# Kernel tuning notes

Hardware: AMD Instinct MI355X
Metric: run time of the kernel (lower is better)

The kernel has to match this reference:

```python
import jax, jax.numpy as jnp
import numpy as np

D = 2048   # embed_dim
E = 128    # expand_ratio = head dim
H = D // E # num heads = 16
C = 64     # chunk size for the chunked linear-attention scan
EPS = 1e-6


def setup_inputs() -> dict:
    key = jax.random.key(0)
    ks = jax.random.split(key, 6)
    b, n = 2, 2048
    s = 0.02
    x = jax.random.normal(ks[0], (b, n, D), jnp.float32)
    Wq = (jax.random.normal(ks[1], (D, D), jnp.float32) * s)
    Wk = (jax.random.normal(ks[2], (D, D), jnp.float32) * s)
    Wv = (jax.random.normal(ks[3], (D, D), jnp.float32) * s)
    Wf = (jax.random.normal(ks[4], (D, H), jnp.float32) * s)
    Wo = (jax.random.normal(ks[5], (D, D), jnp.float32) * s)
    norm_w = jnp.ones((D,), jnp.float32)
    return {"x": x, "Wq": Wq, "Wk": Wk, "Wv": Wv, "Wf": Wf, "Wo": Wo, "norm_w": norm_w}


def _lightning_scalar_decay(q, k, v, ld):
    # q,k,v: [b,n,H,E], ld: [b,n,H] log decay per head per step.
    # Recurrence: S_t = exp(ld_t) * S_{t-1} + k_t^T v_t ; o_t = q_t @ S_t
    b, n, h, e = q.shape
    nc = n // C
    qc = q.reshape(b, nc, C, h, e)
    kc = k.reshape(b, nc, C, h, e)
    vc = v.reshape(b, nc, C, h, e)
    ldc = ld.reshape(b, nc, C, h)
    cum = jnp.cumsum(ldc, axis=2)          # inclusive within-chunk log decay [b,nc,C,h]
    tot = cum[:, :, -1, :]                 # [b,nc,h]

    # intra-chunk: scores[i,j] = (q_i . k_j) * exp(L_i - L_j), j <= i
    Lh = cum.transpose(0, 1, 3, 2)         # [b,nc,h,C]
    decay = jnp.exp(Lh[..., :, None] - Lh[..., None, :])  # [b,nc,h,C,C]
    mask = jnp.tril(jnp.ones((C, C), bool))
    scores = jnp.einsum('bmihe,bmjhe->bmhij', qc, kc) * decay
    scores = jnp.where(mask, scores, 0.0)
    o_intra = jnp.einsum('bmhij,bmjhe->bmihe', scores, vc)

    # inter-chunk: carried recurrent state S [b,h,e,e]
    def step(S, inp):
        q_c, k_c, v_c, cum_c, tot_c = inp  # [b,C,h,e],...,[b,C,h],[b,h]
        o = jnp.einsum('bihe,bhef->bihf', q_c * jnp.exp(cum_c)[..., None], S)
        kd = k_c * jnp.exp(tot_c[:, None, :] - cum_c)[..., None]
        S_new = S * jnp.exp(tot_c)[:, :, None, None] + jnp.einsum('bihe,bihf->bhef', kd, v_c)
        return S_new, o

    xs = (qc.transpose(1, 0, 2, 3, 4), kc.transpose(1, 0, 2, 3, 4),
          vc.transpose(1, 0, 2, 3, 4), cum.transpose(1, 0, 2, 3), tot.transpose(1, 0, 2))
    S0 = jnp.zeros((b, h, e, e), q.dtype)
    S_final, o_inter = jax.lax.scan(step, S0, xs)
    o_inter = o_inter.transpose(1, 0, 2, 3, 4)  # [b,nc,C,h,e]
    return (o_intra + o_inter).reshape(b, n, h * e), S_final


def reference(x, Wq, Wk, Wv, Wf, Wo, norm_w):
    b, n, d = x.shape
    q = jax.nn.silu(x @ Wq).reshape(b, n, H, E)
    k = jax.nn.silu(x @ Wk).reshape(b, n, H, E)
    v = (x @ Wv).reshape(b, n, H, E)
    ld = jax.nn.log_sigmoid(x @ Wf)  # [b,n,H]
    o, _ = _lightning_scalar_decay(q, k, v, ld)
    # RMSNorm over full embed dim
    o = o * jax.lax.rsqrt(jnp.mean(o * o, axis=-1, keepdims=True) + EPS) * norm_w
    return o @ Wo
```

## Files before the change

### kernel.cpp

```cpp
#include <hip/hip_runtime.h>
#include <hip/hip_bf16.h>
#include <stdint.h>

#define D_ 2048
#define E_ 128
#define H_ 16
#define NB_ 2
#define NSEQ_ 2048
#define NTOK_ 4096
#define NCH_ 32

typedef short bf16s;
typedef __attribute__((ext_vector_type(8))) short bf16x8;
typedef __attribute__((ext_vector_type(4))) float f32x4;

__device__ __forceinline__ short f2b(float f) {
  __hip_bfloat16 h = __float2bfloat16(f);
  return *reinterpret_cast<short*>(&h);
}
__device__ __forceinline__ float b2f(short s) {
  __hip_bfloat16 h;
  *reinterpret_cast<short*>(&h) = s;
  return __bfloat162float(h);
}

__device__ __forceinline__ void gload_lds16(const void* g, void* l) {
  __builtin_amdgcn_global_load_lds(
      (__attribute__((address_space(1))) void*)(const_cast<void*>(g)),
      (__attribute__((address_space(3))) void*)(l), 16, 0, 0);
}

__global__ __launch_bounds__(256)
void cvt_bf16(const float* __restrict__ x, bf16s* __restrict__ y) {
  const size_t i = (size_t)blockIdx.x * 256 + threadIdx.x;
  const float4 a = ((const float4*)x)[i * 2];
  const float4 b = ((const float4*)x)[i * 2 + 1];
  bf16x8 o;
  o[0] = f2b(a.x); o[1] = f2b(a.y); o[2] = f2b(a.z); o[3] = f2b(a.w);
  o[4] = f2b(b.x); o[5] = f2b(b.y); o[6] = f2b(b.z); o[7] = f2b(b.w);
  *(bf16x8*)&y[i * 8] = o;
}

__global__ __launch_bounds__(256)
void transpose_w(const float* __restrict__ Wq, const float* __restrict__ Wk,
                 const float* __restrict__ Wv, const float* __restrict__ Wo,
                 const float* __restrict__ nw, bf16s* __restrict__ WqT,
                 bf16s* __restrict__ WkT, bf16s* __restrict__ WvT,
                 bf16s* __restrict__ WoT) {
  const float* src; bf16s* dst;
  if (blockIdx.z == 0)      { src = Wq; dst = WqT; }
  else if (blockIdx.z == 1) { src = Wk; dst = WkT; }
  else if (blockIdx.z == 2) { src = Wv; dst = WvT; }
  else                      { src = Wo; dst = WoT; }
  __shared__ float tile[64][65];
  const int n0 = blockIdx.x * 64, k0 = blockIdx.y * 64;
  const int t = threadIdx.x;
  const int tr = t >> 6, tc = t & 63;
#pragma unroll
  for (int rr = 0; rr < 16; ++rr) {
    const int row = rr * 4 + tr;
    tile[row][tc] = src[(size_t)(k0 + row) * D_ + n0 + tc];
  }
  __syncthreads();
  const float wk = (blockIdx.z == 3) ? nw[k0 + tc] : 1.f;
#pragma unroll
  for (int rr = 0; rr < 16; ++rr) {
    const int row = rr * 4 + tr;
    dst[(size_t)(n0 + row) * D_ + k0 + tc] = f2b(tile[tc][row] * wk);
  }
}

__global__ __launch_bounds__(256)
void ld_gemm(const float* __restrict__ x, const float* __restrict__ Wf,
             float* __restrict__ ldb) {
  const int t = threadIdx.x;
  const int col = t & 15;
  const int tok = blockIdx.x * 16 + (t >> 4);
  const float4* xr = (const float4*)(x + (size_t)tok * D_);
  float s = 0.f;
#pragma unroll 4
  for (int kk = 0; kk < D_ / 4; ++kk) {
    const float4 xv = xr[kk];
    const int k4 = kk * 4;
    s += xv.x * Wf[(k4 + 0) * H_ + col];
    s += xv.y * Wf[(k4 + 1) * H_ + col];
    s += xv.z * Wf[(k4 + 2) * H_ + col];
    s += xv.w * Wf[(k4 + 3) * H_ + col];
  }
  const float m = fminf(s, 0.f);
  ldb[(size_t)tok * H_ + col] = m - log1pf(__expf(-fabsf(s)));
}

template <typename OT>
__device__ __forceinline__ void gemm_body(const bf16s* __restrict__ A,
                                          const bf16s* __restrict__ Bt,
                                          OT* __restrict__ Cm, int bm, int bn,
                                          int act, const float* __restrict__ rs) {
  constexpr int BK = 32;
  __shared__ bf16s As[128 * BK];
  __shared__ bf16s Bs[128 * BK];
  const int t = threadIdx.x;
  const int w = t >> 6, l = t & 63;
  const int wm = w >> 1, wn = w & 1;
  const int lr = l & 15, lk = l >> 4;
  const int sr4 = l >> 2, sc = l & 3;
  f32x4 acc[4][4] = {};

  const size_t abase = (size_t)(bm * 128) * D_;
  const size_t bbase = (size_t)(bn * 128) * D_;

  for (int k0 = 0; k0 < D_; k0 += BK) {
    __syncthreads();
#pragma unroll
    for (int j = 0; j < 2; ++j) {
      const int row0 = j * 64 + w * 16;
      const int row = row0 + sr4;
      const int cs = sc ^ ((row >> 1) & 3);
      gload_lds16(&A[abase + (size_t)row * D_ + k0 + cs * 8], &As[row0 * BK]);
      gload_lds16(&Bt[bbase + (size_t)row * D_ + k0 + cs * 8], &Bs[row0 * BK]);
    }
    __syncthreads();
    bf16x8 af[4], bfr[4];
#pragma unroll
    for (int tm = 0; tm < 4; ++tm) {
      const int row = wm * 64 + tm * 16 + lr;
      af[tm] = *(const bf16x8*)&As[row * BK + (lk ^ ((row >> 1) & 3)) * 8];
    }
#pragma unroll
    for (int tn = 0; tn < 4; ++tn) {
      const int row = wn * 64 + tn * 16 + lr;
      bfr[tn] = *(const bf16x8*)&Bs[row * BK + (lk ^ ((row >> 1) & 3)) * 8];
    }
#pragma unroll
    for (int tm = 0; tm < 4; ++tm)
#pragma unroll
      for (int tn = 0; tn < 4; ++tn)
        acc[tm][tn] = __builtin_amdgcn_mfma_f32_16x16x32_bf16(
            af[tm], bfr[tn], acc[tm][tn], 0, 0, 0);
  }

#pragma unroll
  for (int tm = 0; tm < 4; ++tm) {
    const int rowb = bm * 128 + wm * 64 + tm * 16 + lk * 4;
#pragma unroll
    for (int tn = 0; tn < 4; ++tn) {
      const int col = bn * 128 + wn * 64 + tn * 16 + lr;
#pragma unroll
      for (int r = 0; r < 4; ++r) {
        float vv = acc[tm][tn][r];
        if (act) vv = vv / (1.f + __expf(-vv));
        if constexpr (sizeof(OT) == 2) {
          Cm[(size_t)(rowb + r) * D_ + col] = f2b(vv);
        } else {
          vv *= rs[rowb + r];
          Cm[(size_t)(rowb + r) * D_ + col] = vv;
        }
      }
    }
  }
}

__global__ __launch_bounds__(256, 4)
void gemm_qkv(const bf16s* __restrict__ xb, const bf16s* __restrict__ WqT,
              const bf16s* __restrict__ WkT, const bf16s* __restrict__ WvT,
              bf16s* __restrict__ qb, bf16s* __restrict__ kb,
              bf16s* __restrict__ vb) {
  const int orig = blockIdx.x;
  const int lin = (orig & 7) * 192 + (orig >> 3);
  const int bm = lin & 31;
  const int bnz = lin >> 5;
  const int z = bnz >> 4, bn = bnz & 15;
  const bf16s* Bt; bf16s* out; int act;
  if (z == 0)      { Bt = WqT; out = qb; act = 1; }
  else if (z == 1) { Bt = WkT; out = kb; act = 1; }
  else             { Bt = WvT; out = vb; act = 0; }
  gemm_body<bf16s>(xb, Bt, out, bm, bn, act, nullptr);
}

__global__ __launch_bounds__(256, 4)
void gemm_out(const bf16s* __restrict__ A, const bf16s* __restrict__ Bt,
              const float* __restrict__ rs, float* __restrict__ out) {
  const int orig = blockIdx.x;
  const int lin = (orig & 7) * 64 + (orig >> 3);
  const int bm = lin & 31;
  const int bn = lin >> 5;
  gemm_body<float>(A, Bt, out, bm, bn, 0, rs);
}

__global__ __launch_bounds__(256)
void chunk_state(const bf16s* __restrict__ k, const bf16s* __restrict__ v,
                 const float* __restrict__ ldp, bf16s* __restrict__ Mbuf,
                 float* __restrict__ totb) {
  const int c = blockIdx.x, bh = blockIdx.y;
  const int b = bh >> 4, h = bh & 15;
  const int t = threadIdx.x;
  const int w = t >> 6, l = t & 63;
  const int lr = l & 15, lk = l >> 4;

  __shared__ bf16s Kt[64 * 128];
  __shared__ bf16s Vn[64 * 128];
  __shared__ bf16s KdT[128 * 64];
  __shared__ bf16s VtT[128 * 64];
  __shared__ float cumS[64];
  char* cKt = (char*)Kt; char* cVn = (char*)Vn;
  char* cKdT = (char*)KdT; char* cVtT = (char*)VtT;

  const size_t grow0 = (size_t)b * NSEQ_ + c * 64;
#pragma unroll
  for (int j = 0; j < 4; ++j) {
    const int lrow = w * 16 + j * 4 + (l >> 4);
    const int ck = (l & 15) ^ (lrow & 7);
    const size_t goff = (grow0 + lrow) * D_ + h * E_ + ck * 8;
    const int lbase = (w * 16 + j * 4) * 128;
    gload_lds16(&k[goff], &Kt[lbase]);
    gload_lds16(&v[goff], &Vn[lbase]);
  }
  if (w == 0) {
    float val = ldp[(grow0 + l) * H_ + h];
#pragma unroll
    for (int off = 1; off < 64; off <<= 1) {
      float pv = __shfl_up(val, off);
      if (l >= off) val += pv;
    }
    cumS[l] = val;
  }
  __syncthreads();
  const float tot = cumS[63];
  if (t == 0) totb[bh * NCH_ + c] = tot;

#pragma unroll
  for (int it = 0; it < 4; ++it) {
    const int task = t + it * 256;
    const int i = task >> 4, cx = task & 15;
    const int sb = i * 256 + ((cx * 16) ^ ((i & 7) << 4));
    bf16x8 vv = *(const bf16x8*)(cVn + sb);
    bf16x8 kk8 = *(const bf16x8*)(cKt + sb);
    const float sE = __expf(tot - cumS[i]);
#pragma unroll
    for (int jj = 0; jj < 8; ++jj) {
      const int e = cx * 8 + jj;
      const int db = e * 128 + ((i * 2) ^ ((e & 7) << 4));
      *(bf16s*)(cVtT + db) = vv[jj];
      *(bf16s*)(cKdT + db) = f2b(b2f(kk8[jj]) * sE);
    }
  }
  __syncthreads();

  const int wm = w >> 1, wn = w & 1;
  f32x4 acc[4][4] = {};
#pragma unroll
  for (int kk2 = 0; kk2 < 2; ++kk2) {
    const int cb = (kk2 * 32 + lk * 8) * 2;
    bf16x8 af[4], bfr[4];
#pragma unroll
    for (int tm = 0; tm < 4; ++tm) {
      const int fr = wm * 64 + tm * 16 + lr;
      af[tm] = *(const bf16x8*)(cVtT + fr * 128 + (cb ^ ((fr & 7) << 4)));
    }
#pragma unroll
    for (int tn = 0; tn < 4; ++tn) {
      const int er = wn * 64 + tn * 16 + lr;
      bfr[tn] = *(const bf16x8*)(cKdT + er * 128 + (cb ^ ((er & 7) << 4)));
    }
#pragma unroll
    for (int tm = 0; tm < 4; ++tm)
#pragma unroll
      for (int tn = 0; tn < 4; ++tn)
        acc[tm][tn] = __builtin_amdgcn_mfma_f32_16x16x32_bf16(
            af[tm], bfr[tn], acc[tm][tn], 0, 0, 0);
  }
  const size_t mb = (size_t)(bh * NCH_ + c) * 128 * 128;
#pragma unroll
  for (int tm = 0; tm < 4; ++tm) {
#pragma unroll
    for (int tn = 0; tn < 4; ++tn) {
#pragma unroll
      for (int r = 0; r < 4; ++r) {
        const int f = wm * 64 + tm * 16 + lk * 4 + r;
        const int e = wn * 64 + tn * 16 + lr;
        Mbuf[mb + f * 128 + e] = f2b(acc[tm][tn][r]);
      }
    }
  }
}

__global__ __launch_bounds__(256)
void state_scan(const bf16s* __restrict__ Mbuf, const float* __restrict__ totb,
                bf16s* __restrict__ Sbuf) {
  const int sl = blockIdx.x;
  const int bh = blockIdx.y;
  const int t = threadIdx.x;
  const int fr = sl * 16 + (t >> 4);
  const int e0 = (t & 15) * 8;
  const size_t base = ((size_t)(bh * NCH_) * 128 + fr) * 128 + e0;
  const size_t cstride = 128 * 128;
  __shared__ float tots[NCH_];
  if (t < NCH_) tots[t] = totb[bh * NCH_ + t];
  __syncthreads();
  float acc[8] = {};
  bf16x8 m0 = *(const bf16x8*)&Mbuf[base + 0 * cstride];
  bf16x8 m1 = *(const bf16x8*)&Mbuf[base + 1 * cstride];
  bf16x8 m2 = *(const bf16x8*)&Mbuf[base + 2 * cstride];
  bf16x8 m3 = *(const bf16x8*)&Mbuf[base + 3 * cstride];
#pragma unroll
  for (int c = 0; c < NCH_; ++c) {
    bf16x8 sv;
#pragma unroll
    for (int j = 0; j < 8; ++j) sv[j] = f2b(acc[j]);
    *(bf16x8*)&Sbuf[base + (size_t)c * cstride] = sv;
    const bf16x8 mc = ((c & 3) == 0) ? m0 : ((c & 3) == 1) ? m1
                     : ((c & 3) == 2) ? m2 : m3;
    const float dt = __expf(tots[c]);
#pragma unroll
    for (int j = 0; j < 8; ++j) acc[j] = acc[j] * dt + b2f(mc[j]);
    if (c + 4 < NCH_) {
      const bf16x8 mn = *(const bf16x8*)&Mbuf[base + (size_t)(c + 4) * cstride];
      if ((c & 3) == 0) m0 = mn;
      else if ((c & 3) == 1) m1 = mn;
      else if ((c & 3) == 2) m2 = mn;
      else m3 = mn;
    }
  }
}

__global__ __launch_bounds__(256)
void attn_out(const bf16s* __restrict__ q, const bf16s* __restrict__ k,
              const bf16s* __restrict__ v, const float* __restrict__ ldp,
              const bf16s* __restrict__ Sbuf, bf16s* __restrict__ o) {
  const int c = blockIdx.x, bh = blockIdx.y;
  const int b = bh >> 4, h = bh & 15;
  const int t = threadIdx.x;
  const int w = t >> 6, l = t & 63;
  const int lr = l & 15, lk = l >> 4;

  __shared__ bf16s Qt[64 * 128];
  __shared__ bf16s Kt[64 * 128];
  __shared__ bf16s Vn[64 * 128];
  __shared__ bf16s VtT[128 * 64];
  __shared__ bf16s Pm[64 * 64];
  __shared__ float cumS[64];
  char* cQt = (char*)Qt; char* cKt = (char*)Kt; char* cVn = (char*)Vn;
  char* cVtT = (char*)VtT; char* cPm = (char*)Pm;

  const size_t grow0 = (size_t)b * NSEQ_ + c * 64;
  const size_t sbase = (size_t)(bh * NCH_ + c) * 128 * 128;
  const bf16x8* Sp = (const bf16x8*)&Sbuf[sbase];
#pragma unroll
  for (int j = 0; j < 4; ++j) {
    const int lrow = w * 16 + j * 4 + (l >> 4);
    const int ck = (l & 15) ^ (lrow & 7);
    const size_t goff = (grow0 + lrow) * D_ + h * E_ + ck * 8;
    const int lbase = (w * 16 + j * 4) * 128;
    gload_lds16(&q[goff], &Qt[lbase]);
    gload_lds16(&k[goff], &Kt[lbase]);
    gload_lds16(&v[goff], &Vn[lbase]);
  }
  if (w == 0) {
    float val = ldp[(grow0 + l) * H_ + h];
#pragma unroll
    for (int off = 1; off < 64; off <<= 1) {
      float pv = __shfl_up(val, off);
      if (l >= off) val += pv;
    }
    cumS[l] = val;
  }
  __syncthreads();

#pragma unroll
  for (int it = 0; it < 4; ++it) {
    const int task = t + it * 256;
    const int i = task >> 4, cx = task & 15;
    const int sb = i * 256 + ((cx * 16) ^ ((i & 7) << 4));
    bf16x8 vv = *(const bf16x8*)(cVn + sb);
#pragma unroll
    for (int jj = 0; jj < 8; ++jj) {
      const int e = cx * 8 + jj;
      const int db = e * 128 + ((i * 2) ^ ((e & 7) << 4));
      *(bf16s*)(cVtT + db) = vv[jj];
    }
  }

  f32x4 accs[4] = {};
  f32x4 acco[8] = {};
#pragma unroll
  for (int kk = 0; kk < 4; ++kk) {
    const int cb = (kk * 32 + lk * 8) * 2;
    const int ar = w * 16 + lr;
    bf16x8 aq = *(const bf16x8*)(cQt + ar * 256 + (cb ^ ((ar & 7) << 4)));
#pragma unroll
    for (int tn = 0; tn < 4; ++tn) {
      const int br = tn * 16 + lr;
      bf16x8 bk = *(const bf16x8*)(cKt + br * 256 + (cb ^ ((br & 7) << 4)));
      accs[tn] = __builtin_amdgcn_mfma_f32_16x16x32_bf16(aq, bk, accs[tn], 0, 0, 0);
    }
#pragma unroll
    for (int tf = 0; tf < 8; ++tf) {
      bf16x8 bs = Sp[(tf * 16 + lr) * 16 + kk * 4 + lk];
      acco[tf] = __builtin_amdgcn_mfma_f32_16x16x32_bf16(aq, bs, acco[tf], 0, 0, 0);
    }
  }
#pragma unroll
  for (int r = 0; r < 4; ++r) {
    const float gI = __expf(cumS[w * 16 + lk * 4 + r]);
#pragma unroll
    for (int tf = 0; tf < 8; ++tf) acco[tf][r] *= gI;
  }
#pragma unroll
  for (int tn = 0; tn < 4; ++tn) {
    const int j = tn * 16 + lr;
    const float cj = cumS[j];
#pragma unroll
    for (int r = 0; r < 4; ++r) {
      const int i = w * 16 + lk * 4 + r;
      const float sv = (j <= i) ? accs[tn][r] * __expf(cumS[i] - cj) : 0.f;
      *(bf16s*)(cPm + i * 128 + ((j * 2) ^ ((i & 7) << 4))) = f2b(sv);
    }
  }
  __syncthreads();

#pragma unroll
  for (int kk2 = 0; kk2 < 2; ++kk2) {
    const int cb = (kk2 * 32 + lk * 8) * 2;
    const int pr = w * 16 + lr;
    bf16x8 ap = *(const bf16x8*)(cPm + pr * 128 + (cb ^ ((pr & 7) << 4)));
#pragma unroll
    for (int tf = 0; tf < 8; ++tf) {
      const int fr = tf * 16 + lr;
      bf16x8 bv = *(const bf16x8*)(cVtT + fr * 128 + (cb ^ ((fr & 7) << 4)));
      acco[tf] = __builtin_amdgcn_mfma_f32_16x16x32_bf16(ap, bv, acco[tf], 0, 0, 0);
    }
  }
#pragma unroll
  for (int tf = 0; tf < 8; ++tf) {
#pragma unroll
    for (int r = 0; r < 4; ++r) {
      const int i = w * 16 + lk * 4 + r;
      o[(grow0 + i) * D_ + h * E_ + tf * 16 + lr] = f2b(acco[tf][r]);
    }
  }
}

__global__ __launch_bounds__(256)
void rms_scale(const bf16s* __restrict__ o, float* __restrict__ sout) {
  const int tok = blockIdx.x;
  const int t = threadIdx.x;
  bf16x8 vv = *(const bf16x8*)&o[(size_t)tok * D_ + t * 8];
  float s = 0.f;
#pragma unroll
  for (int j = 0; j < 8; ++j) { const float f = b2f(vv[j]); s += f * f; }
#pragma unroll
  for (int off2 = 32; off2 > 0; off2 >>= 1) s += __shfl_down(s, off2);
  __shared__ float wsum[4];
  if ((t & 63) == 0) wsum[t >> 6] = s;
  __syncthreads();
  if (t == 0)
    sout[tok] = rsqrtf((wsum[0] + wsum[1] + wsum[2] + wsum[3]) * (1.f / D_) +
                       1e-6f);
}

extern "C" void kernel_launch(void* const* d_in, const int* in_sizes, int n_in,
                              void* d_out, int out_size, void* d_ws,
                              size_t ws_size, hipStream_t stream) {
  (void)in_sizes; (void)n_in; (void)out_size;
  const float* x  = (const float*)d_in[0];
  const float* Wq = (const float*)d_in[1];
  const float* Wk = (const float*)d_in[2];
  const float* Wv = (const float*)d_in[3];
  const float* Wf = (const float*)d_in[4];
  const float* Wo = (const float*)d_in[5];
  const float* nw = (const float*)d_in[6];
  float* out = (float*)d_out;

  char* ws = (char*)d_ws;
  const size_t MB = 1024 * 1024;
  bf16s* xb   = (bf16s*)(ws + 0);
  bf16s* WqT  = (bf16s*)(ws + 16 * MB);
  bf16s* WkT  = (bf16s*)(ws + 24 * MB);
  bf16s* WvT  = (bf16s*)(ws + 32 * MB);
  bf16s* Sbuf = (bf16s*)(ws + 0);
  float* totb = (float*)(ws + 32 * MB);
  bf16s* WoT  = (bf16s*)(ws + 40 * MB);
  bf16s* qb   = (bf16s*)(ws + 48 * MB);
  bf16s* kb   = (bf16s*)(ws + 64 * MB);
  bf16s* vb   = (bf16s*)(ws + 80 * MB);
  bf16s* ob   = (bf16s*)(ws + 96 * MB);
  bf16s* Mbuf = (bf16s*)(ws + 112 * MB);
  float* ldb  = (float*)(ws + 144 * MB);
  float* rsb  = (float*)(ws + 145 * MB);
  if (146 * MB > ws_size) return;

  cvt_bf16<<<NTOK_ * D_ / 8 / 256, 256, 0, stream>>>(x, xb);
  transpose_w<<<dim3(32, 32, 4), 256, 0, stream>>>(Wq, Wk, Wv, Wo, nw, WqT,
                                                   WkT, WvT, WoT);
  ld_gemm<<<NTOK_ / 16, 256, 0, stream>>>(x, Wf, ldb);
  gemm_qkv<<<1536, 256, 0, stream>>>(xb, WqT, WkT, WvT, qb, kb, vb);
  chunk_state<<<dim3(NCH_, NB_ * H_), 256, 0, stream>>>(kb, vb, ldb, Mbuf, totb);
  state_scan<<<dim3(8, NB_ * H_), 256, 0, stream>>>(Mbuf, totb, Sbuf);
  attn_out<<<dim3(NCH_, NB_ * H_), 256, 0, stream>>>(qb, kb, vb, ldb, Sbuf, ob);
  rms_scale<<<NTOK_, 256, 0, stream>>>(ob, rsb);
  gemm_out<<<512, 256, 0, stream>>>(ob, WoT, rsb, out);
}
```

Measured before the change: 317.9 us.

## Enlarge GEMM tiles to 128x256 with each wave covering all rows

The shared GEMM body now computes 128x256 output tiles. Each of the four waves handles a 128x64 slab, with 8x4 MFMA accumulators per lane instead of 4x4. This raises MFMA work per LDS fragment load and halves the block count. In exchange it doubles register use, lowers the occupancy bound to 2, and replaces the swizzled block ordering with a plain grid, which may hurt L2 locality and wave-level parallelism.

Measured after the change: 361.0 us. +13.6%, slower.

```diff
diff --git a/kernel.cpp b/kernel.cpp
--- a/kernel.cpp
+++ b/kernel.cpp
@@ -98,16 +98,15 @@
                                           int act, const float* __restrict__ rs) {
   constexpr int BK = 32;
   __shared__ bf16s As[128 * BK];
-  __shared__ bf16s Bs[128 * BK];
+  __shared__ bf16s Bs[256 * BK];
   const int t = threadIdx.x;
   const int w = t >> 6, l = t & 63;
-  const int wm = w >> 1, wn = w & 1;
   const int lr = l & 15, lk = l >> 4;
   const int sr4 = l >> 2, sc = l & 3;
-  f32x4 acc[4][4] = {};
+  f32x4 acc[8][4] = {};
 
   const size_t abase = (size_t)(bm * 128) * D_;
-  const size_t bbase = (size_t)(bn * 128) * D_;
+  const size_t bbase = (size_t)(bn * 256) * D_;
 
   for (int k0 = 0; k0 < D_; k0 += BK) {
     __syncthreads();
@@ -117,22 +116,28 @@
       const int row = row0 + sr4;
       const int cs = sc ^ ((row >> 1) & 3);
       gload_lds16(&A[abase + (size_t)row * D_ + k0 + cs * 8], &As[row0 * BK]);
+    }
+#pragma unroll
+    for (int j = 0; j < 4; ++j) {
+      const int row0 = j * 64 + w * 16;
+      const int row = row0 + sr4;
+      const int cs = sc ^ ((row >> 1) & 3);
       gload_lds16(&Bt[bbase + (size_t)row * D_ + k0 + cs * 8], &Bs[row0 * BK]);
     }
     __syncthreads();
-    bf16x8 af[4], bfr[4];
-#pragma unroll
-    for (int tm = 0; tm < 4; ++tm) {
-      const int row = wm * 64 + tm * 16 + lr;
+    bf16x8 af[8], bfr[4];
+#pragma unroll
+    for (int tm = 0; tm < 8; ++tm) {
+      const int row = tm * 16 + lr;
       af[tm] = *(const bf16x8*)&As[row * BK + (lk ^ ((row >> 1) & 3)) * 8];
     }
 #pragma unroll
     for (int tn = 0; tn < 4; ++tn) {
-      const int row = wn * 64 + tn * 16 + lr;
+      const int row = w * 64 + tn * 16 + lr;
       bfr[tn] = *(const bf16x8*)&Bs[row * BK + (lk ^ ((row >> 1) & 3)) * 8];
     }
 #pragma unroll
-    for (int tm = 0; tm < 4; ++tm)
+    for (int tm = 0; tm < 8; ++tm)
 #pragma unroll
       for (int tn = 0; tn < 4; ++tn)
         acc[tm][tn] = __builtin_amdgcn_mfma_f32_16x16x32_bf16(
@@ -140,11 +145,11 @@
   }
 
 #pragma unroll
-  for (int tm = 0; tm < 4; ++tm) {
-    const int rowb = bm * 128 + wm * 64 + tm * 16 + lk * 4;
+  for (int tm = 0; tm < 8; ++tm) {
+    const int rowb = bm * 128 + tm * 16 + lk * 4;
 #pragma unroll
     for (int tn = 0; tn < 4; ++tn) {
-      const int col = bn * 128 + wn * 64 + tn * 16 + lr;
+      const int col = bn * 256 + w * 64 + tn * 16 + lr;
 #pragma unroll
       for (int r = 0; r < 4; ++r) {
         float vv = acc[tm][tn][r];
@@ -160,16 +165,12 @@
   }
 }
 
-__global__ __launch_bounds__(256, 4)
+__global__ __launch_bounds__(256, 2)
 void gemm_qkv(const bf16s* __restrict__ xb, const bf16s* __restrict__ WqT,
               const bf16s* __restrict__ WkT, const bf16s* __restrict__ WvT,
               bf16s* __restrict__ qb, bf16s* __restrict__ kb,
               bf16s* __restrict__ vb) {
-  const int orig = blockIdx.x;
-  const int lin = (orig & 7) * 192 + (orig >> 3);
-  const int bm = lin & 31;
-  const int bnz = lin >> 5;
-  const int z = bnz >> 4, bn = bnz & 15;
+  const int bn = blockIdx.x, bm = blockIdx.y, z = blockIdx.z;
   const bf16s* Bt; bf16s* out; int act;
   if (z == 0)      { Bt = WqT; out = qb; act = 1; }
   else if (z == 1) { Bt = WkT; out = kb; act = 1; }
@@ -177,14 +178,10 @@
   gemm_body<bf16s>(xb, Bt, out, bm, bn, act, nullptr);
 }
 
-__global__ __launch_bounds__(256, 4)
+__global__ __launch_bounds__(256, 2)
 void gemm_out(const bf16s* __restrict__ A, const bf16s* __restrict__ Bt,
               const float* __restrict__ rs, float* __restrict__ out) {
-  const int orig = blockIdx.x;
-  const int lin = (orig & 7) * 64 + (orig >> 3);
-  const int bm = lin & 31;
-  const int bn = lin >> 5;
-  gemm_body<float>(A, Bt, out, bm, bn, 0, rs);
+  gemm_body<float>(A, Bt, out, blockIdx.y, blockIdx.x, 0, rs);
 }
 
 __global__ __launch_bounds__(256)
@@ -493,10 +490,10 @@
   transpose_w<<<dim3(32, 32, 4), 256, 0, stream>>>(Wq, Wk, Wv, Wo, nw, WqT,
                                                    WkT, WvT, WoT);
   ld_gemm<<<NTOK_ / 16, 256, 0, stream>>>(x, Wf, ldb);
-  gemm_qkv<<<1536, 256, 0, stream>>>(xb, WqT, WkT, WvT, qb, kb, vb);
+  gemm_qkv<<<dim3(8, 32, 3), 256, 0, stream>>>(xb, WqT, WkT, WvT, qb, kb, vb);
   chunk_state<<<dim3(NCH_, NB_ * H_), 256, 0, stream>>>(kb, vb, ldb, Mbuf, totb);
   state_scan<<<dim3(8, NB_ * H_), 256, 0, stream>>>(Mbuf, totb, Sbuf);
   attn_out<<<dim3(NCH_, NB_ * H_), 256, 0, stream>>>(qb, kb, vb, ldb, Sbuf, ob);
   rms_scale<<<NTOK_, 256, 0, stream>>>(ob, rsb);
-  gemm_out<<<512, 256, 0, stream>>>(ob, WoT, rsb, out);
-}
+  gemm_out<<<dim3(8, 32), 256, 0, stream>>>(ob, WoT, rsb, out);
+}
```
